# Kernel optimization log

Hardware: AMD Instinct MI355X
Metric: run time of the kernel (lower is better)

The kernel has to match this reference:

```python
import jax, jax.numpy as jnp
import numpy as np

FDIM, HDIM, DIM = 512, 512, 256
B, N = 64, 4096


def setup_inputs() -> dict:
    key = jax.random.key(0)
    k1, k2, k3, k4, k5 = jax.random.split(key, 5)
    image_features = jax.random.normal(k1, (B, N, FDIM), dtype=jnp.float32)
    hidden_state = jax.random.normal(k2, (B, HDIM), dtype=jnp.float32)
    # nn.Linear weights: stored [out, in]; y = x @ W.T
    W_img = jax.random.normal(k3, (DIM, FDIM), dtype=jnp.float32) * (FDIM ** -0.5)
    W_hid = jax.random.normal(k4, (DIM, HDIM), dtype=jnp.float32) * (HDIM ** -0.5)
    W_score = jax.random.normal(k5, (1, DIM), dtype=jnp.float32) * (DIM ** -0.5)
    return {"image_features": image_features, "hidden_state": hidden_state,
            "W_img": W_img, "W_hid": W_hid, "W_score": W_score}


def reference(image_features, hidden_state, W_img, W_hid, W_score):
    # proj_image: [B, N, D]
    proj_image = jnp.einsum('bnf,df->bnd', image_features, W_img)
    # proj_hidden: [B, 1, D]
    proj_hidden = jnp.einsum('bh,dh->bd', hidden_state, W_hid)[:, None, :]
    combined = jnp.tanh(proj_image + proj_hidden)            # [B, N, D]
    scores = jnp.einsum('bnd,d->bn', combined, W_score[0])   # [B, N]
    weights = jax.nn.softmax(scores, axis=-1)                # [B, N]
    context = jnp.einsum('bn,bnf->bf', weights, image_features)  # [B, F]
    return (context, weights)
```

## Files before the change

### kernel.cpp

```cpp
#include <hip/hip_runtime.h>
#include <hip/hip_bf16.h>

#define B_ 64
#define N_ 4096
#define F_ 512
#define D_ 256
#define BM 64
#define APAD 520
#define NCHUNK (N_ / BM)
#define GT 16
#define NBLK (B_ * NCHUNK / GT)

typedef __attribute__((ext_vector_type(8))) short short8;
typedef __attribute__((ext_vector_type(4))) float f32x4;

__device__ __forceinline__ unsigned short f2bf(float f) {
  unsigned int u = __float_as_uint(f);
  u += 0x7FFFu + ((u >> 16) & 1u);
  return (unsigned short)(u >> 16);
}

__device__ __forceinline__ unsigned int pk2bf(float x, float y) {
  float2 f; f.x = x; f.y = y;
  __hip_bfloat162 h = __float22bfloat162_rn(f);
  union { __hip_bfloat162 h2; unsigned int u; } cv; cv.h2 = h;
  return cv.u;
}

__device__ __forceinline__ float fast_tanh(float x) {
  float e = __expf(-2.0f * fabsf(x));
  float t = (1.0f - e) / (1.0f + e);
  return copysignf(t, x);
}

#define SBAR                                                                   \
  do {                                                                         \
    __builtin_amdgcn_sched_barrier(0);                                         \
    __builtin_amdgcn_s_barrier();                                              \
    __builtin_amdgcn_sched_barrier(0);                                         \
  } while (0)

#define LGKM0                                                                  \
  do {                                                                         \
    asm volatile("s_waitcnt lgkmcnt(0)" ::: "memory");                         \
    __builtin_amdgcn_sched_barrier(0);                                         \
  } while (0)

__global__ void prep_w_kernel(const float* __restrict__ Wimg,
                              unsigned short* __restrict__ wfrag) {
  int d = blockIdx.x;
  int f = threadIdx.x;
  int q = f >> 5, lg = (f >> 3) & 3, e = f & 7;
  int lr = d & 15, d16 = d >> 4;
  int lane = lg * 16 + lr;
  int idx = ((q * 16 + d16) * 64 + lane) * 8 + e;
  wfrag[idx] = f2bf(Wimg[d * F_ + f]);
}

__global__ void prep_ph_kernel(const float* __restrict__ hid,
                               const float* __restrict__ Whid,
                               float* __restrict__ ph) {
  int b = blockIdx.x, d = threadIdx.x;
  const float4* hv = (const float4*)(hid + b * F_);
  const float4* wv = (const float4*)(Whid + d * F_);
  float acc = 0.f;
#pragma unroll 4
  for (int i = 0; i < 128; i++) {
    float4 h = hv[i], w = wv[i];
    acc += h.x * w.x + h.y * w.y + h.z * w.z + h.w * w.w;
  }
  ph[b * D_ + d] = acc;
}

__global__ __launch_bounds__(512, 2) void fused_kernel(
    const float* __restrict__ feat, const unsigned short* __restrict__ wfrag,
    const float* __restrict__ ph, const float* __restrict__ wscore,
    float* __restrict__ expw, float2* __restrict__ meta,
    float* __restrict__ part) {
  __shared__ unsigned short Afull[BM * APAD];
  __shared__ float red[BM][8];
  __shared__ float sbuf[BM];
  __shared__ float ewf[BM];

  int tid = threadIdx.x;
  int lane = tid & 63, wn = tid >> 6;
  int lr = lane & 15, lg = lane >> 4;

  int blk = blockIdx.x;
  int b = blk >> 2, j = blk & 3;

  short8 bq[16][2];
#pragma unroll
  for (int q = 0; q < 16; q++)
#pragma unroll
    for (int n = 0; n < 2; n++)
      bq[q][n] = *(const short8*)(wfrag +
          (size_t)((q * 16 + wn * 2 + n) * 64 + lane) * 8);

  float ph2[2], ws2[2];
#pragma unroll
  for (int n = 0; n < 2; n++) {
    int d = wn * 32 + n * 16 + lr;
    ph2[n] = ph[b * D_ + d];
    ws2[n] = wscore[d];
  }

  int row_s = tid >> 3, c0 = (tid & 7) * 8;
  const float* arow = feat + ((size_t)b * N_ + (size_t)j * GT * BM) * F_;

#define LOADS(buf, ptr, kt_)                                                   \
  do {                                                                         \
    buf##_0 = *(const float4*)((ptr) + (size_t)row_s * F_ + (kt_)*64 + c0);    \
    buf##_1 = *(const float4*)((ptr) + (size_t)row_s * F_ + (kt_)*64 + c0 + 4);\
  } while (0)

#define CVTW(buf, kt_)                                                         \
  do {                                                                         \
    uint4 wv; wv.x = pk2bf(buf##_0.x, buf##_0.y);                              \
    wv.y = pk2bf(buf##_0.z, buf##_0.w);                                        \
    wv.z = pk2bf(buf##_1.x, buf##_1.y);                                        \
    wv.w = pk2bf(buf##_1.z, buf##_1.w);                                        \
    *(uint4*)(Afull + row_s * APAD + (kt_)*64 + c0) = wv;                      \
  } while (0)

#define QQ(q_)                                                                 \
  do {                                                                         \
    short8 af0 = *(const short8*)(Afull + (0 * 16 + lr) * APAD + (q_)*32 + lg * 8); \
    short8 af1 = *(const short8*)(Afull + (1 * 16 + lr) * APAD + (q_)*32 + lg * 8); \
    short8 af2 = *(const short8*)(Afull + (2 * 16 + lr) * APAD + (q_)*32 + lg * 8); \
    short8 af3 = *(const short8*)(Afull + (3 * 16 + lr) * APAD + (q_)*32 + lg * 8); \
    acc[0][0] = __builtin_amdgcn_mfma_f32_16x16x32_bf16(af0, bq[q_][0], acc[0][0], 0, 0, 0); \
    acc[0][1] = __builtin_amdgcn_mfma_f32_16x16x32_bf16(af0, bq[q_][1], acc[0][1], 0, 0, 0); \
    acc[1][0] = __builtin_amdgcn_mfma_f32_16x16x32_bf16(af1, bq[q_][0], acc[1][0], 0, 0, 0); \
    acc[1][1] = __builtin_amdgcn_mfma_f32_16x16x32_bf16(af1, bq[q_][1], acc[1][1], 0, 0, 0); \
    acc[2][0] = __builtin_amdgcn_mfma_f32_16x16x32_bf16(af2, bq[q_][0], acc[2][0], 0, 0, 0); \
    acc[2][1] = __builtin_amdgcn_mfma_f32_16x16x32_bf16(af2, bq[q_][1], acc[2][1], 0, 0, 0); \
    acc[3][0] = __builtin_amdgcn_mfma_f32_16x16x32_bf16(af3, bq[q_][0], acc[3][0], 0, 0, 0); \
    acc[3][1] = __builtin_amdgcn_mfma_f32_16x16x32_bf16(af3, bq[q_][1], acc[3][1], 0, 0, 0); \
  } while (0)

  float4 rs0_0, rs0_1, rs1_0, rs1_1;
  LOADS(rs0, arow, 0);
  LOADS(rs1, arow, 1);

#pragma unroll 1
  for (int t = 0; t < GT; t++) {
    const float* nrow = (t < GT - 1) ? (arow + (size_t)BM * F_) : arow;
    f32x4 acc[4][2];
#pragma unroll
    for (int m = 0; m < 4; m++)
#pragma unroll
      for (int n = 0; n < 2; n++) acc[m][n] = (f32x4)0.f;

    CVTW(rs0, 0); LGKM0; SBAR;
    LOADS(rs0, arow, 2); QQ(0);  QQ(1);  CVTW(rs1, 1); LGKM0; SBAR;
    LOADS(rs1, arow, 3); QQ(2);  QQ(3);  CVTW(rs0, 2); LGKM0; SBAR;
    LOADS(rs0, arow, 4); QQ(4);  QQ(5);  CVTW(rs1, 3); LGKM0; SBAR;
    LOADS(rs1, arow, 5); QQ(6);  QQ(7);  CVTW(rs0, 4); LGKM0; SBAR;
    LOADS(rs0, arow, 6); QQ(8);  QQ(9);  CVTW(rs1, 5); LGKM0; SBAR;
    LOADS(rs1, arow, 7); QQ(10); QQ(11); CVTW(rs0, 6); LGKM0; SBAR;
    LOADS(rs0, nrow, 0); QQ(12); QQ(13); CVTW(rs1, 7); LGKM0; SBAR;
    LOADS(rs1, nrow, 1); QQ(14); QQ(15);

#pragma unroll
    for (int m = 0; m < 4; m++) {
#pragma unroll
      for (int jj = 0; jj < 4; jj++) {
        float p = fast_tanh(acc[m][0][jj] + ph2[0]) * ws2[0] +
                  fast_tanh(acc[m][1][jj] + ph2[1]) * ws2[1];
        p += __shfl_xor(p, 1);
        p += __shfl_xor(p, 2);
        p += __shfl_xor(p, 4);
        p += __shfl_xor(p, 8);
        if (lr == 0) red[m * 16 + lg * 4 + jj][wn] = p;
      }
    }
    __syncthreads();
    if (tid < BM) {
      float s = 0.f;
#pragma unroll
      for (int w = 0; w < 8; w++) s += red[tid][w];
      sbuf[tid] = s;
    }
    __syncthreads();

    int tile = j * GT + t;
    int n0 = tile * BM;
    float mb = -1e30f;
#pragma unroll
    for (int r = 0; r < BM; r++) mb = fmaxf(mb, sbuf[r]);
    if (tid < BM) {
      float e = __expf(sbuf[tid] - mb);
      ewf[tid] = e;
      expw[b * N_ + n0 + tid] = e;
      float l = e;
#pragma unroll
      for (int o = 1; o < 64; o <<= 1) l += __shfl_xor(l, o);
      if (tid == 0) meta[b * NCHUNK + tile] = make_float2(mb, l);
    }
    __syncthreads();

    {
      float a = 0.f;
#pragma unroll 8
      for (int r = 0; r < BM; r++) {
        unsigned short v = Afull[r * APAD + tid];
        a += ewf[r] * __uint_as_float((unsigned int)v << 16);
      }
      part[(size_t)(b * NCHUNK + tile) * F_ + tid] = a;
    }
    __syncthreads();

    arow = nrow;
  }
}

__global__ void finalize_kernel(const float* __restrict__ part,
                                const float2* __restrict__ meta,
                                const float* __restrict__ expw,
                                float* __restrict__ ctx,
                                float* __restrict__ wout) {
  __shared__ float sm[NCHUNK], sl[NCHUNK], se[NCHUNK];
  int b = blockIdx.x, t = threadIdx.x;
  if (t < NCHUNK) {
    float2 ml = meta[b * NCHUNK + t];
    sm[t] = ml.x;
    sl[t] = ml.y;
  }
  __syncthreads();
  float M = -1e30f;
#pragma unroll 8
  for (int i = 0; i < NCHUNK; i++) M = fmaxf(M, sm[i]);
  float Z = 0.f;
#pragma unroll 8
  for (int i = 0; i < NCHUNK; i++) Z += sl[i] * __expf(sm[i] - M);
  if (t < NCHUNK) se[t] = __expf(sm[t] - M);
  __syncthreads();
  float invZ = 1.0f / Z;
  float acc = 0.f;
#pragma unroll 8
  for (int i = 0; i < NCHUNK; i++) acc += part[(size_t)(b * NCHUNK + i) * F_ + t] * se[i];
  ctx[b * F_ + t] = acc * invZ;
#pragma unroll
  for (int k = 0; k < 8; k++) {
    int n = k * 512 + t;
    wout[b * N_ + n] = expw[b * N_ + n] * se[n >> 6] * invZ;
  }
}

extern "C" void kernel_launch(void* const* d_in, const int* in_sizes, int n_in,
                              void* d_out, int out_size, void* d_ws, size_t ws_size,
                              hipStream_t stream) {
  const float* feat   = (const float*)d_in[0];
  const float* hid    = (const float*)d_in[1];
  const float* Wimg   = (const float*)d_in[2];
  const float* Whid   = (const float*)d_in[3];
  const float* Wscore = (const float*)d_in[4];

  float* ctx  = (float*)d_out;
  float* wout = (float*)d_out + B_ * F_;

  unsigned short* wfrag = (unsigned short*)d_ws;
  float*  ph    = (float*)((char*)d_ws + 262144);
  float*  expw  = (float*)((char*)d_ws + 327680);
  float2* meta  = (float2*)((char*)d_ws + 1376256);
  float*  part  = (float*)((char*)d_ws + 1409024);

  prep_w_kernel<<<D_, F_, 0, stream>>>(Wimg, wfrag);
  prep_ph_kernel<<<B_, D_, 0, stream>>>(hid, Whid, ph);
  fused_kernel<<<NBLK, 512, 0, stream>>>(feat, wfrag, ph, Wscore, expw, meta, part);
  finalize_kernel<<<B_, 512, 0, stream>>>(part, meta, expw, ctx, wout);
}
```

Baseline: 237.0 us.

## Halve tile rows, double-buffer LDS, overlap epilogue with next tile's MFMA

```diff
diff --git a/kernel.cpp b/kernel.cpp
--- a/kernel.cpp
+++ b/kernel.cpp
@@ -5,11 +5,12 @@
 #define N_ 4096
 #define F_ 512
 #define D_ 256
-#define BM 64
+#define BM 32
 #define APAD 520
 #define NCHUNK (N_ / BM)
-#define GT 16
-#define NBLK (B_ * NCHUNK / GT)
+#define GT 4
+#define NGRP (NCHUNK / GT)
+#define NBLK (B_ * NGRP)
 
 typedef __attribute__((ext_vector_type(8))) short short8;
 typedef __attribute__((ext_vector_type(4))) float f32x4;
@@ -27,9 +28,16 @@
   return cv.u;
 }
 
+__device__ __forceinline__ float rcp_f(float x) {
+  float r; asm("v_rcp_f32 %0, %1" : "=v"(r) : "v"(x)); return r;
+}
+__device__ __forceinline__ float exp2_f(float x) {
+  float r; asm("v_exp_f32 %0, %1" : "=v"(r) : "v"(x)); return r;
+}
 __device__ __forceinline__ float fast_tanh(float x) {
-  float e = __expf(-2.0f * fabsf(x));
-  float t = (1.0f - e) / (1.0f + e);
+  float a = fabsf(x);
+  float e = exp2_f(-2.885390082f * a);
+  float t = (1.f - e) * rcp_f(1.f + e);
   return copysignf(t, x);
 }
 
@@ -77,141 +85,147 @@
     const float* __restrict__ ph, const float* __restrict__ wscore,
     float* __restrict__ expw, float2* __restrict__ meta,
     float* __restrict__ part) {
-  __shared__ unsigned short Afull[BM * APAD];
+  __shared__ unsigned short Afull[2][BM * APAD];
   __shared__ float red[BM][8];
   __shared__ float sbuf[BM];
   __shared__ float ewf[BM];
 
   int tid = threadIdx.x;
-  int lane = tid & 63, wn = tid >> 6;
+  int lane = tid & 63, wv = tid >> 6;
   int lr = lane & 15, lg = lane >> 4;
+  int wv2 = wv * 2;
 
   int blk = blockIdx.x;
-  int b = blk >> 2, j = blk & 3;
-
-  short8 bq[16][2];
-#pragma unroll
-  for (int q = 0; q < 16; q++)
-#pragma unroll
-    for (int n = 0; n < 2; n++)
-      bq[q][n] = *(const short8*)(wfrag +
-          (size_t)((q * 16 + wn * 2 + n) * 64 + lane) * 8);
+  int b = blk >> 5, g = blk & 31;
+
+  const float* base = feat + ((size_t)b * N_ + (size_t)g * GT * BM) * F_;
 
   float ph2[2], ws2[2];
 #pragma unroll
   for (int n = 0; n < 2; n++) {
-    int d = wn * 32 + n * 16 + lr;
+    int d = wv * 32 + n * 16 + lr;
     ph2[n] = ph[b * D_ + d];
     ws2[n] = wscore[d];
   }
 
-  int row_s = tid >> 3, c0 = (tid & 7) * 8;
-  const float* arow = feat + ((size_t)b * N_ + (size_t)j * GT * BM) * F_;
-
-#define LOADS(buf, ptr, kt_)                                                   \
-  do {                                                                         \
-    buf##_0 = *(const float4*)((ptr) + (size_t)row_s * F_ + (kt_)*64 + c0);    \
-    buf##_1 = *(const float4*)((ptr) + (size_t)row_s * F_ + (kt_)*64 + c0 + 4);\
-  } while (0)
-
-#define CVTW(buf, kt_)                                                         \
-  do {                                                                         \
-    uint4 wv; wv.x = pk2bf(buf##_0.x, buf##_0.y);                              \
-    wv.y = pk2bf(buf##_0.z, buf##_0.w);                                        \
-    wv.z = pk2bf(buf##_1.x, buf##_1.y);                                        \
-    wv.w = pk2bf(buf##_1.z, buf##_1.w);                                        \
-    *(uint4*)(Afull + row_s * APAD + (kt_)*64 + c0) = wv;                      \
-  } while (0)
-
-#define QQ(q_)                                                                 \
-  do {                                                                         \
-    short8 af0 = *(const short8*)(Afull + (0 * 16 + lr) * APAD + (q_)*32 + lg * 8); \
-    short8 af1 = *(const short8*)(Afull + (1 * 16 + lr) * APAD + (q_)*32 + lg * 8); \
-    short8 af2 = *(const short8*)(Afull + (2 * 16 + lr) * APAD + (q_)*32 + lg * 8); \
-    short8 af3 = *(const short8*)(Afull + (3 * 16 + lr) * APAD + (q_)*32 + lg * 8); \
-    acc[0][0] = __builtin_amdgcn_mfma_f32_16x16x32_bf16(af0, bq[q_][0], acc[0][0], 0, 0, 0); \
-    acc[0][1] = __builtin_amdgcn_mfma_f32_16x16x32_bf16(af0, bq[q_][1], acc[0][1], 0, 0, 0); \
-    acc[1][0] = __builtin_amdgcn_mfma_f32_16x16x32_bf16(af1, bq[q_][0], acc[1][0], 0, 0, 0); \
-    acc[1][1] = __builtin_amdgcn_mfma_f32_16x16x32_bf16(af1, bq[q_][1], acc[1][1], 0, 0, 0); \
-    acc[2][0] = __builtin_amdgcn_mfma_f32_16x16x32_bf16(af2, bq[q_][0], acc[2][0], 0, 0, 0); \
-    acc[2][1] = __builtin_amdgcn_mfma_f32_16x16x32_bf16(af2, bq[q_][1], acc[2][1], 0, 0, 0); \
-    acc[3][0] = __builtin_amdgcn_mfma_f32_16x16x32_bf16(af3, bq[q_][0], acc[3][0], 0, 0, 0); \
-    acc[3][1] = __builtin_amdgcn_mfma_f32_16x16x32_bf16(af3, bq[q_][1], acc[3][1], 0, 0, 0); \
-  } while (0)
-
-  float4 rs0_0, rs0_1, rs1_0, rs1_1;
-  LOADS(rs0, arow, 0);
-  LOADS(rs1, arow, 1);
+  int prow = tid >> 5;
+  int pcol = tid & 31;
+
+  float4 rs0[2], rs1[2];
+
+#define LOADP(buf, ptr, p_)                                                    \
+  do {                                                                         \
+    buf[0] = *(const float4*)((ptr) + (size_t)prow * F_ + (p_)*128 + pcol * 4);\
+    buf[1] = *(const float4*)((ptr) + (size_t)(prow + 16) * F_ + (p_)*128 + pcol * 4); \
+  } while (0)
+
+#define CVTP(ab_, buf, p_)                                                     \
+  do {                                                                         \
+    _Pragma("unroll") for (int i = 0; i < 2; i++) {                            \
+      uint2 w_;                                                                \
+      w_.x = pk2bf(buf[i].x, buf[i].y);                                        \
+      w_.y = pk2bf(buf[i].z, buf[i].w);                                        \
+      *(uint2*)(&Afull[ab_][(prow + i * 16) * APAD + (p_)*128 + pcol * 4]) = w_; \
+    }                                                                          \
+  } while (0)
+
+  f32x4 acc00 = (f32x4)0.f, acc01 = (f32x4)0.f, acc10 = (f32x4)0.f, acc11 = (f32x4)0.f;
+  f32x4 accP00 = (f32x4)0.f, accP01 = (f32x4)0.f, accP10 = (f32x4)0.f, accP11 = (f32x4)0.f;
+
+#define QQ(ab_, q_)                                                            \
+  do {                                                                         \
+    short8 bf0 = *(const short8*)(wfrag + (size_t)(((q_)*16 + wv2 + 0) * 64 + lane) * 8); \
+    short8 bf1 = *(const short8*)(wfrag + (size_t)(((q_)*16 + wv2 + 1) * 64 + lane) * 8); \
+    short8 af0 = *(const short8*)(&Afull[ab_][lr * APAD + (q_)*32 + lg * 8]);  \
+    short8 af1 = *(const short8*)(&Afull[ab_][(16 + lr) * APAD + (q_)*32 + lg * 8]); \
+    acc00 = __builtin_amdgcn_mfma_f32_16x16x32_bf16(af0, bf0, acc00, 0, 0, 0); \
+    acc01 = __builtin_amdgcn_mfma_f32_16x16x32_bf16(af0, bf1, acc01, 0, 0, 0); \
+    acc10 = __builtin_amdgcn_mfma_f32_16x16x32_bf16(af1, bf0, acc10, 0, 0, 0); \
+    acc11 = __builtin_amdgcn_mfma_f32_16x16x32_bf16(af1, bf1, acc11, 0, 0, 0); \
+  } while (0)
+
+#define QQ4(ab_, p_) { QQ(ab_, (p_)*4 + 0); QQ(ab_, (p_)*4 + 1); QQ(ab_, (p_)*4 + 2); QQ(ab_, (p_)*4 + 3); }
+
+#define EPI0()                                                                 \
+  do {                                                                         \
+    _Pragma("unroll") for (int j = 0; j < 4; j++) {                            \
+      float p0 = fast_tanh(accP00[j] + ph2[0]) * ws2[0] +                      \
+                 fast_tanh(accP01[j] + ph2[1]) * ws2[1];                       \
+      float p1 = fast_tanh(accP10[j] + ph2[0]) * ws2[0] +                      \
+                 fast_tanh(accP11[j] + ph2[1]) * ws2[1];                       \
+      p0 += __shfl_xor(p0, 1); p0 += __shfl_xor(p0, 2);                        \
+      p0 += __shfl_xor(p0, 4); p0 += __shfl_xor(p0, 8);                        \
+      p1 += __shfl_xor(p1, 1); p1 += __shfl_xor(p1, 2);                        \
+      p1 += __shfl_xor(p1, 4); p1 += __shfl_xor(p1, 8);                        \
+      if (lr == 0) {                                                           \
+        red[lg * 4 + j][wv] = p0;                                              \
+        red[16 + lg * 4 + j][wv] = p1;                                         \
+      }                                                                        \
+    }                                                                          \
+  } while (0)
+
+#define EPI1()                                                                 \
+  do {                                                                         \
+    if (tid < BM)                                                              \
+      sbuf[tid] = red[tid][0] + red[tid][1] + red[tid][2] + red[tid][3] +      \
+                  red[tid][4] + red[tid][5] + red[tid][6] + red[tid][7];       \
+  } while (0)
+
+#define EPI2(cp_)                                                              \
+  do {                                                                         \
+    float mb_ = -1e30f;                                                        \
+    _Pragma("unroll") for (int r = 0; r < BM; r++) mb_ = fmaxf(mb_, sbuf[r]);  \
+    if (tid < BM) {                                                            \
+      float e_ = __expf(sbuf[tid] - mb_);                                      \
+      ewf[tid] = e_;                                                           \
+      expw[b * N_ + (cp_)*BM + tid] = e_;                                      \
+      float l_ = e_;                                                           \
+      l_ += __shfl_xor(l_, 1); l_ += __shfl_xor(l_, 2);                        \
+      l_ += __shfl_xor(l_, 4); l_ += __shfl_xor(l_, 8);                        \
+      l_ += __shfl_xor(l_, 16);                                                \
+      if (tid == 0) meta[b * NCHUNK + (cp_)] = make_float2(mb_, l_);           \
+    }                                                                          \
+  } while (0)
+
+#define EPI3(cp_, pb_)                                                         \
+  do {                                                                         \
+    float a_ = 0.f;                                                            \
+    int ca_ = tid & ~1;                                                        \
+    _Pragma("unroll") for (int r = 0; r < BM; r++) {                           \
+      unsigned int v_ = *(const unsigned int*)(&Afull[pb_][r * APAD + ca_]);   \
+      a_ += ewf[r] * __uint_as_float((tid & 1) ? (v_ & 0xffff0000u) : (v_ << 16)); \
+    }                                                                          \
+    part[(size_t)(b * NCHUNK + (cp_)) * F_ + tid] = a_;                        \
+  } while (0)
+
+  LOADP(rs0, base, 0);
+  LOADP(rs1, base, 1);
 
 #pragma unroll 1
   for (int t = 0; t < GT; t++) {
+    int ab = t & 1, pb = ab ^ 1;
+    const float* arow = base + (size_t)t * BM * F_;
     const float* nrow = (t < GT - 1) ? (arow + (size_t)BM * F_) : arow;
-    f32x4 acc[4][2];
-#pragma unroll
-    for (int m = 0; m < 4; m++)
-#pragma unroll
-      for (int n = 0; n < 2; n++) acc[m][n] = (f32x4)0.f;
-
-    CVTW(rs0, 0); LGKM0; SBAR;
-    LOADS(rs0, arow, 2); QQ(0);  QQ(1);  CVTW(rs1, 1); LGKM0; SBAR;
-    LOADS(rs1, arow, 3); QQ(2);  QQ(3);  CVTW(rs0, 2); LGKM0; SBAR;
-    LOADS(rs0, arow, 4); QQ(4);  QQ(5);  CVTW(rs1, 3); LGKM0; SBAR;
-    LOADS(rs1, arow, 5); QQ(6);  QQ(7);  CVTW(rs0, 4); LGKM0; SBAR;
-    LOADS(rs0, arow, 6); QQ(8);  QQ(9);  CVTW(rs1, 5); LGKM0; SBAR;
-    LOADS(rs1, arow, 7); QQ(10); QQ(11); CVTW(rs0, 6); LGKM0; SBAR;
-    LOADS(rs0, nrow, 0); QQ(12); QQ(13); CVTW(rs1, 7); LGKM0; SBAR;
-    LOADS(rs1, nrow, 1); QQ(14); QQ(15);
-
-#pragma unroll
-    for (int m = 0; m < 4; m++) {
-#pragma unroll
-      for (int jj = 0; jj < 4; jj++) {
-        float p = fast_tanh(acc[m][0][jj] + ph2[0]) * ws2[0] +
-                  fast_tanh(acc[m][1][jj] + ph2[1]) * ws2[1];
-        p += __shfl_xor(p, 1);
-        p += __shfl_xor(p, 2);
-        p += __shfl_xor(p, 4);
-        p += __shfl_xor(p, 8);
-        if (lr == 0) red[m * 16 + lg * 4 + jj][wn] = p;
-      }
-    }
-    __syncthreads();
-    if (tid < BM) {
-      float s = 0.f;
-#pragma unroll
-      for (int w = 0; w < 8; w++) s += red[tid][w];
-      sbuf[tid] = s;
-    }
-    __syncthreads();
-
-    int tile = j * GT + t;
-    int n0 = tile * BM;
-    float mb = -1e30f;
-#pragma unroll
-    for (int r = 0; r < BM; r++) mb = fmaxf(mb, sbuf[r]);
-    if (tid < BM) {
-      float e = __expf(sbuf[tid] - mb);
-      ewf[tid] = e;
-      expw[b * N_ + n0 + tid] = e;
-      float l = e;
-#pragma unroll
-      for (int o = 1; o < 64; o <<= 1) l += __shfl_xor(l, o);
-      if (tid == 0) meta[b * NCHUNK + tile] = make_float2(mb, l);
-    }
-    __syncthreads();
-
-    {
-      float a = 0.f;
-#pragma unroll 8
-      for (int r = 0; r < BM; r++) {
-        unsigned short v = Afull[r * APAD + tid];
-        a += ewf[r] * __uint_as_float((unsigned int)v << 16);
-      }
-      part[(size_t)(b * NCHUNK + tile) * F_ + tid] = a;
-    }
-    __syncthreads();
-
-    arow = nrow;
+    int cp = g * GT + t - 1;
+    bool hp = (t > 0);
+
+    CVTP(ab, rs0, 0); LGKM0; SBAR;
+    LOADP(rs0, arow, 2); if (hp) EPI0();        QQ4(ab, 0); CVTP(ab, rs1, 1); LGKM0; SBAR;
+    LOADP(rs1, arow, 3); if (hp) EPI1();        QQ4(ab, 1); CVTP(ab, rs0, 2); LGKM0; SBAR;
+    LOADP(rs0, nrow, 0); if (hp) EPI2(cp);      QQ4(ab, 2); CVTP(ab, rs1, 3); LGKM0; SBAR;
+    LOADP(rs1, nrow, 1); if (hp) EPI3(cp, pb);  QQ4(ab, 3); SBAR;
+
+    accP00 = acc00; accP01 = acc01; accP10 = acc10; accP11 = acc11;
+    acc00 = (f32x4)0.f; acc01 = (f32x4)0.f; acc10 = (f32x4)0.f; acc11 = (f32x4)0.f;
+  }
+
+  {
+    int cp = g * GT + GT - 1;
+    int pb = (GT - 1) & 1;
+    EPI0(); LGKM0; SBAR;
+    EPI1(); LGKM0; SBAR;
+    EPI2(cp); LGKM0; SBAR;
+    EPI3(cp, pb);
   }
 }
 
@@ -244,7 +258,7 @@
 #pragma unroll
   for (int k = 0; k < 8; k++) {
     int n = k * 512 + t;
-    wout[b * N_ + n] = expw[b * N_ + n] * se[n >> 6] * invZ;
+    wout[b * N_ + n] = expw[b * N_ + n] * se[n >> 5] * invZ;
   }
 }
 
@@ -264,7 +278,7 @@
   float*  ph    = (float*)((char*)d_ws + 262144);
   float*  expw  = (float*)((char*)d_ws + 327680);
   float2* meta  = (float2*)((char*)d_ws + 1376256);
-  float*  part  = (float*)((char*)d_ws + 1409024);
+  float*  part  = (float*)((char*)d_ws + 1441792);
 
   prep_w_kernel<<<D_, F_, 0, stream>>>(Wimg, wfrag);
   prep_ph_kernel<<<B_, D_, 0, stream>>>(hid, Whid, ph);
```

Result: slower. 251.0 us (+5.9%).
